# Optimization experiments

Hardware: AMD Instinct MI355X
Metric: run time of the kernel (lower is better)

## Reference

```python
import jax, jax.numpy as jnp
import numpy as np

B, S, DIM, HDIM = 8, 1024, 1024, 128
H = DIM // HDIM  # 8 heads
GN_EPS = 1e-3    # keras GroupNormalization default epsilon


def group_norm(y, gamma, beta, groups, eps=GN_EPS):
    # keras GroupNormalization on [B,S,C]: reshape to [B,S,groups,C//groups],
    # normalize over all axes except batch and group axis -> axes (1,3).
    b, s, c = y.shape
    g = y.reshape(b, s, groups, c // groups)
    mean = g.mean(axis=(1, 3), keepdims=True)
    var = g.var(axis=(1, 3), keepdims=True)
    g = (g - mean) * jax.lax.rsqrt(var + eps)
    return g.reshape(b, s, c) * gamma + beta


def setup_inputs() -> dict:
    key = jax.random.key(0)
    ks = jax.random.split(key, 7)
    x = jax.random.normal(ks[0], (B, S, DIM), dtype=jnp.float32)
    sc_h = 1.0 / np.sqrt(HDIM).astype(np.float32)
    sc_d = 1.0 / np.sqrt(DIM).astype(np.float32)
    Wq = jax.random.normal(ks[1], (H, HDIM, HDIM), dtype=jnp.float32) * sc_h
    Wk = jax.random.normal(ks[2], (H, HDIM, HDIM), dtype=jnp.float32) * sc_h
    Wv = jax.random.normal(ks[3], (H, HDIM, HDIM), dtype=jnp.float32) * sc_h
    Wg = jax.random.normal(ks[4], (DIM, DIM), dtype=jnp.float32) * sc_d
    Wo = jax.random.normal(ks[5], (DIM, DIM), dtype=jnp.float32) * sc_d
    gn_gamma = jnp.ones((DIM,), dtype=jnp.float32)
    gn_beta = jnp.zeros((DIM,), dtype=jnp.float32)
    return {"x": x, "Wq": Wq, "Wk": Wk, "Wv": Wv, "Wg": Wg, "Wo": Wo,
            "gn_gamma": gn_gamma, "gn_beta": gn_beta}


def reference(x, Wq, Wk, Wv, Wg, Wo, gn_gamma, gn_beta):
    b, s, c = x.shape
    h, hd = Wq.shape[0], Wq.shape[1]
    # gating branch: W = ReLU(x @ Wg)
    Wgate = jax.nn.relu(jnp.einsum('bsc,cd->bsd', x, Wg))
    # split channels into heads: [B,S,H,hd]
    xh = x.reshape(b, s, h, hd)
    Q = jnp.einsum('bshd,hde->bhse', xh, Wq)
    K = jnp.einsum('bshd,hde->bhse', xh, Wk)
    V = jnp.einsum('bshd,hde->bhse', xh, Wv)
    # per-head decay mask D[h,i,j] = gamma_h ** (i - j) (full, non-causal as in source)
    idx = jnp.arange(s, dtype=jnp.float32)
    gammas = 1.0 - 2.0 ** (-5.0 - jnp.arange(h, dtype=jnp.float32))  # [H]
    decay = gammas[:, None, None] ** (idx[None, :, None] - idx[None, None, :])  # [H,S,S]
    scores = jnp.einsum('bhsd,bhtd->bhst', Q, K) * decay[None]
    ret = jnp.einsum('bhst,bhtd->bhsd', scores, V)       # [B,H,S,hd]
    y = ret.transpose(0, 2, 1, 3).reshape(b, s, c)        # concat heads
    Y = group_norm(y, gn_gamma, gn_beta, groups=hd)       # groups = hdim (keras arg)
    return jnp.einsum('bsc,cd->bsd', Wgate * Y, Wo)
```

## Files before the change

kernel.cpp:

```cpp
#include <hip/hip_runtime.h>

#define BB 8
#define SS 1024
#define DD 1024
#define HH 8
#define HD 128
#define GN_EPS 1e-3f

typedef __attribute__((ext_vector_type(8))) short bf16x8;
typedef __attribute__((ext_vector_type(4))) float f32x4;

__device__ __forceinline__ short f2bf(float f) {
    unsigned u = __float_as_uint(f);
    return (short)((u + 0x7fffu + ((u >> 16) & 1u)) >> 16);
}
__device__ __forceinline__ float bf2f(short s) {
    return __uint_as_float(((unsigned)(unsigned short)s) << 16);
}

__device__ __forceinline__ void gload16(const void* g, void* l) {
    __builtin_amdgcn_global_load_lds((const __attribute__((address_space(1))) void*)g,
                                     (__attribute__((address_space(3))) void*)l, 16, 0, 0);
}

__device__ __forceinline__ void stage_tile(const short* __restrict__ G, size_t ld, int k0,
                                           short* lds, int wid, int lane) {
#pragma unroll
    for (int i = 0; i < 2; i++) {
        const int seg = wid * 2 + i;
        const int row = seg * 8 + (lane >> 3);
        const int chunk = (lane & 7) ^ (lane >> 3);
        gload16(G + (size_t)row * ld + k0 + chunk * 8, lds + seg * 512);
    }
}

__device__ __forceinline__ void gemm_tile_g(
    const short* __restrict__ A, size_t ldA,
    const short* __restrict__ B, size_t ldB,
    int K, short* As, short* Bs, f32x4 acc[4][2])
{
    const int tid = threadIdx.x, lane = tid & 63, wid = tid >> 6;
    const int wr = (wid >> 2) * 64, wc = (wid & 3) * 32;
    const int fr = lane & 15, fc = lane >> 4;
    const int rsw = fr & 7;
#pragma unroll
    for (int i = 0; i < 4; i++)
#pragma unroll
        for (int j = 0; j < 2; j++) acc[i][j] = (f32x4){0.f, 0.f, 0.f, 0.f};

    const int nt = K >> 6;
    stage_tile(A, ldA, 0, As, wid, lane);
    stage_tile(B, ldB, 0, Bs, wid, lane);
    if (nt > 1) {
        stage_tile(A, ldA, 64, As + 8192, wid, lane);
        stage_tile(B, ldB, 64, Bs + 8192, wid, lane);
    }
    for (int t = 0; t < nt; t++) {
        if (t + 1 < nt) asm volatile("s_waitcnt vmcnt(4)" ::: "memory");
        else            asm volatile("s_waitcnt vmcnt(0)" ::: "memory");
        __builtin_amdgcn_s_barrier();
        __builtin_amdgcn_sched_barrier(0);
        const int cur = t & 1;
        const short* as = As + (cur << 13);
        const short* bs = Bs + (cur << 13);
#pragma unroll
        for (int half = 0; half < 2; half++) {
            const int slot = ((half * 4 + fc) ^ rsw) << 3;
            bf16x8 af[4], bfv[2];
#pragma unroll
            for (int i = 0; i < 4; i++) af[i] = *(const bf16x8*)&as[(wr + i * 16 + fr) * 64 + slot];
#pragma unroll
            for (int j = 0; j < 2; j++) bfv[j] = *(const bf16x8*)&bs[(wc + j * 16 + fr) * 64 + slot];
#pragma unroll
            for (int i = 0; i < 4; i++)
#pragma unroll
                for (int j = 0; j < 2; j++)
                    acc[i][j] = __builtin_amdgcn_mfma_f32_16x16x32_bf16(af[i], bfv[j], acc[i][j], 0, 0, 0);
        }
        __builtin_amdgcn_sched_barrier(0);
        asm volatile("s_waitcnt lgkmcnt(0)" ::: "memory");
        __builtin_amdgcn_s_barrier();
        if (t + 2 < nt) {
            stage_tile(A, ldA, (t + 2) << 6, As + (cur << 13), wid, lane);
            stage_tile(B, ldB, (t + 2) << 6, Bs + (cur << 13), wid, lane);
        }
    }
}

__global__ __launch_bounds__(256) void prep(
    const float* __restrict__ x,
    const float* __restrict__ Wq, const float* __restrict__ Wk, const float* __restrict__ Wv,
    const float* __restrict__ Wg, const float* __restrict__ Wo,
    short* __restrict__ xb, short* __restrict__ WgT, short* __restrict__ WoT,
    short* __restrict__ Wt, float* __restrict__ sQ, float* __restrict__ sK,
    float* __restrict__ Sp)
{
    __shared__ float t[32][33];
    int bid = blockIdx.x;
    const int tid = threadIdx.x;
    if (bid < 4096) {
        const size_t i = ((size_t)bid * 256 + tid) * 8;
        float4 a = *(const float4*)&x[i];
        float4 b = *(const float4*)&x[i + 4];
        bf16x8 v;
        v[0] = f2bf(a.x); v[1] = f2bf(a.y); v[2] = f2bf(a.z); v[3] = f2bf(a.w);
        v[4] = f2bf(b.x); v[5] = f2bf(b.y); v[6] = f2bf(b.z); v[7] = f2bf(b.w);
        *(bf16x8*)&xb[i] = v;
        return;
    }
    bid -= 4096;
    if (bid < 2048) {
        const float* __restrict__ S = (bid < 1024) ? Wg : Wo;
        short* __restrict__ D = (bid < 1024) ? WgT : WoT;
        const int tb = bid & 1023;
        const int bx = (tb & 31) * 32, by = (tb >> 5) * 32;
        const int xx = tid & 31, y0 = tid >> 5;
#pragma unroll
        for (int r = 0; r < 32; r += 8) t[y0 + r][xx] = S[(size_t)(by + y0 + r) * 1024 + bx + xx];
        __syncthreads();
#pragma unroll
        for (int r = 0; r < 32; r += 8) D[(size_t)(bx + y0 + r) * 1024 + by + xx] = f2bf(t[xx][y0 + r]);
        return;
    }
    bid -= 2048;
    if (bid < 384) {
        const int ht = bid >> 4, tb = bid & 15;
        const int typ = ht >> 3, h = ht & 7;
        const float* __restrict__ W = (typ == 0 ? Wq : (typ == 1 ? Wk : Wv)) + (size_t)h * HD * HD;
        short* __restrict__ D = Wt + (size_t)ht * HD * HD;
        const int bx = (tb & 3) * 32, by = (tb >> 2) * 32;
        const int xx = tid & 31, y0 = tid >> 5;
#pragma unroll
        for (int r = 0; r < 32; r += 8) t[y0 + r][xx] = W[(by + y0 + r) * HD + bx + xx];
        __syncthreads();
#pragma unroll
        for (int r = 0; r < 32; r += 8) D[(bx + y0 + r) * HD + by + xx] = f2bf(t[xx][y0 + r]);
        return;
    }
    bid -= 384;
    if (bid < 32) {
        const int h = bid >> 2;
        const int s = (bid & 3) * 256 + tid;
        const double gamma = 1.0 - exp2((double)(-5 - h));
        const double lg = log2(gamma);
        sQ[h * SS + s] = (float)exp2(lg * (double)s);
        sK[h * SS + s] = (float)exp2(-lg * (double)s);
        return;
    }
    *(float4*)&Sp[tid * 8] = (float4){0.f, 0.f, 0.f, 0.f};
    *(float4*)&Sp[tid * 8 + 4] = (float4){0.f, 0.f, 0.f, 0.f};
}

__global__ __launch_bounds__(512) void g_qkvgate(
    const short* __restrict__ xb, const short* __restrict__ Wt, const short* __restrict__ WgT,
    const float* __restrict__ sQ, const float* __restrict__ sK,
    short* __restrict__ Qb, short* __restrict__ Ktb, short* __restrict__ Vtb,
    short* __restrict__ gateb)
{
    __shared__ short As[2 * 8192], Bs[2 * 8192];
    f32x4 acc[4][2];
    const int orig = blockIdx.x;
    const int cx = orig & 7, p = orig >> 3;
    const int tid = threadIdx.x, lane = tid & 63, wid = tid >> 6;
    const int wr = (wid >> 2) * 64, wc = (wid & 3) * 32;
    const int r0 = (lane >> 4) * 4, c = lane & 15;

    if (p < 64) {
        const int w2 = cx * 64 + p;
        const int m0 = (w2 >> 3) * 128, n0 = (w2 & 7) * 128;
        gemm_tile_g(xb + (size_t)m0 * DD, DD, WgT + (size_t)n0 * DD, DD, DD, As, Bs, acc);
#pragma unroll
        for (int i = 0; i < 4; i++)
#pragma unroll
            for (int j = 0; j < 2; j++)
#pragma unroll
                for (int r = 0; r < 4; r++)
                    gateb[(size_t)(m0 + wr + i * 16 + r0 + r) * DD + n0 + wc + j * 16 + c] =
                        f2bf(fmaxf(acc[i][j][r], 0.f));
        return;
    }
    const int w = cx * 64 + (p - 64);
    const int mt = w >> 3, h = w & 7;
    const int m0 = mt * 128;
    const int b = m0 >> 10, s0 = m0 & (SS - 1);
    const int bh = (b << 3) + h;
    const short* __restrict__ A = xb + (size_t)m0 * DD + h * HD;

    const int fr = lane & 15, fc = lane >> 4;
    const int rsw = fr & 7;

    stage_tile(A, DD, 0,  As,        wid, lane);
    stage_tile(A, DD, 64, As + 8192, wid, lane);
    stage_tile(Wt + (size_t)h * HD * HD, HD, 0, Bs, wid, lane);
    __syncthreads();

#pragma unroll
    for (int i = 0; i < 4; i++)
#pragma unroll
        for (int j = 0; j < 2; j++) acc[i][j] = (f32x4){0.f, 0.f, 0.f, 0.f};

    int sb = 0;
    for (int st = 0; st < 6; st++) {
        if (st + 1 < 6) {
            const int typn = (st + 1) >> 1, ktn = (st + 1) & 1;
            stage_tile(Wt + (size_t)(typn * 8 + h) * HD * HD, HD, ktn * 64,
                       Bs + ((sb ^ 1) << 13), wid, lane);
        }
        const int kt = st & 1;
        const short* as = As + (kt << 13);
        const short* bs = Bs + (sb << 13);
#pragma unroll
        for (int half = 0; half < 2; half++) {
            const int slot = ((half * 4 + fc) ^ rsw) << 3;
            bf16x8 af[4], bfv[2];
#pragma unroll
            for (int i = 0; i < 4; i++) af[i] = *(const bf16x8*)&as[(wr + i * 16 + fr) * 64 + slot];
#pragma unroll
            for (int j = 0; j < 2; j++) bfv[j] = *(const bf16x8*)&bs[(wc + j * 16 + fr) * 64 + slot];
#pragma unroll
            for (int i = 0; i < 4; i++)
#pragma unroll
                for (int j = 0; j < 2; j++)
                    acc[i][j] = __builtin_amdgcn_mfma_f32_16x16x32_bf16(af[i], bfv[j], acc[i][j], 0, 0, 0);
        }
        __syncthreads();
        sb ^= 1;
        if (kt == 1) {
            const int typ = st >> 1;
            if (typ == 0) {
#pragma unroll
                for (int i = 0; i < 4; i++)
#pragma unroll
                    for (int j = 0; j < 2; j++)
#pragma unroll
                        for (int r = 0; r < 4; r++) {
                            const int s = s0 + wr + i * 16 + r0 + r;
                            Qb[((size_t)bh * SS + s) * HD + wc + j * 16 + c] =
                                f2bf(acc[i][j][r] * sQ[h * SS + s]);
                        }
            } else if (typ == 1) {
                short* __restrict__ Ob = Ktb + (size_t)bh * HD * SS;
#pragma unroll
                for (int i = 0; i < 4; i++)
#pragma unroll
                    for (int j = 0; j < 2; j++) {
                        const int tb = s0 + wr + i * 16 + r0;
                        const int d = wc + j * 16 + c;
                        short4 o;
                        o.x = f2bf(acc[i][j][0] * sK[h * SS + tb + 0]);
                        o.y = f2bf(acc[i][j][1] * sK[h * SS + tb + 1]);
                        o.z = f2bf(acc[i][j][2] * sK[h * SS + tb + 2]);
                        o.w = f2bf(acc[i][j][3] * sK[h * SS + tb + 3]);
                        *(short4*)&Ob[(size_t)d * SS + tb] = o;
                    }
            } else {
                short* __restrict__ Ob = Vtb + (size_t)bh * HD * SS;
#pragma unroll
                for (int i = 0; i < 4; i++)
#pragma unroll
                    for (int j = 0; j < 2; j++) {
                        const int tb = s0 + wr + i * 16 + r0;
                        const int e = wc + j * 16 + c;
                        short4 o;
                        o.x = f2bf(acc[i][j][0]); o.y = f2bf(acc[i][j][1]);
                        o.z = f2bf(acc[i][j][2]); o.w = f2bf(acc[i][j][3]);
                        *(short4*)&Ob[(size_t)e * SS + tb] = o;
                    }
            }
#pragma unroll
            for (int i = 0; i < 4; i++)
#pragma unroll
                for (int j = 0; j < 2; j++) acc[i][j] = (f32x4){0.f, 0.f, 0.f, 0.f};
        }
    }
}

__global__ __launch_bounds__(512) void g_kv(
    const short* __restrict__ Vtb, const short* __restrict__ Ktb, float* __restrict__ Mp)
{
    __shared__ short As[2 * 8192], Bs[2 * 8192];
    f32x4 acc[4][2];
    const int orig = blockIdx.x;
    const int w = (orig & 7) * 16 + (orig >> 3);
    const int chunk = w & 1, bh = w >> 1;
    gemm_tile_g(Vtb + (size_t)bh * HD * SS + chunk * 512, SS,
                Ktb + (size_t)bh * HD * SS + chunk * 512, SS, 512, As, Bs, acc);
    const int tid = threadIdx.x, lane = tid & 63, wid = tid >> 6;
    const int wr = (wid >> 2) * 64, wc = (wid & 3) * 32;
    const int r0 = (lane >> 4) * 4, c = lane & 15;
    float* __restrict__ Ob = Mp + (size_t)w * HD * HD;
#pragma unroll
    for (int i = 0; i < 4; i++)
#pragma unroll
        for (int j = 0; j < 2; j++)
#pragma unroll
            for (int r = 0; r < 4; r++)
                Ob[(size_t)(wr + i * 16 + r0 + r) * HD + wc + j * 16 + c] = acc[i][j][r];
}

__global__ __launch_bounds__(256) void g_mredcvt(const float* __restrict__ Mp, short* __restrict__ Mtb) {
    const size_t i = ((size_t)blockIdx.x * 256 + threadIdx.x) * 8;
    const size_t bh = i >> 14, ij = i & 16383;
    const float* p = Mp + (bh * 2) * 16384 + ij;
    float s[8];
#pragma unroll
    for (int q = 0; q < 8; q++) s[q] = 0.f;
#pragma unroll
    for (int cth = 0; cth < 2; cth++) {
        float4 a = *(const float4*)&p[cth * 16384];
        float4 b = *(const float4*)&p[cth * 16384 + 4];
        s[0] += a.x; s[1] += a.y; s[2] += a.z; s[3] += a.w;
        s[4] += b.x; s[5] += b.y; s[6] += b.z; s[7] += b.w;
    }
    bf16x8 v;
#pragma unroll
    for (int q = 0; q < 8; q++) v[q] = f2bf(s[q]);
    *(bf16x8*)&Mtb[i] = v;
}

__global__ __launch_bounds__(512) void g_qm(
    const short* __restrict__ Qb, const short* __restrict__ Mtb,
    short* __restrict__ retc, float* __restrict__ Sp)
{
    __shared__ short As[2 * 8192], Bs[2 * 8192];
    f32x4 acc[4][2];
    const int orig = blockIdx.x;
    const int w = (orig & 7) * 64 + (orig >> 3);
    const int bh = w >> 3, m0 = (w & 7) * 128;
    const short* __restrict__ A = Qb + ((size_t)bh * SS + m0) * HD;
    const short* __restrict__ Bp = Mtb + (size_t)bh * HD * HD;
    const int tid = threadIdx.x, lane = tid & 63, wid = tid >> 6;
    const int wr = (wid >> 2) * 64, wc = (wid & 3) * 32;
    const int fr = lane & 15, fc = lane >> 4, rsw = fr & 7;
    const int r0 = (lane >> 4) * 4, c = lane & 15;

    stage_tile(A,  HD, 0,  As,        wid, lane);
    stage_tile(A,  HD, 64, As + 8192, wid, lane);
    stage_tile(Bp, HD, 0,  Bs,        wid, lane);
    stage_tile(Bp, HD, 64, Bs + 8192, wid, lane);
#pragma unroll
    for (int i = 0; i < 4; i++)
#pragma unroll
        for (int j = 0; j < 2; j++) acc[i][j] = (f32x4){0.f, 0.f, 0.f, 0.f};
    asm volatile("s_waitcnt vmcnt(0)" ::: "memory");
    __builtin_amdgcn_s_barrier();
    __builtin_amdgcn_sched_barrier(0);
#pragma unroll
    for (int kt = 0; kt < 2; kt++) {
        const short* as = As + (kt << 13);
        const short* bs = Bs + (kt << 13);
#pragma unroll
        for (int half = 0; half < 2; half++) {
            const int slot = ((half * 4 + fc) ^ rsw) << 3;
            bf16x8 af[4], bfv[2];
#pragma unroll
            for (int i = 0; i < 4; i++) af[i] = *(const bf16x8*)&as[(wr + i * 16 + fr) * 64 + slot];
#pragma unroll
            for (int j = 0; j < 2; j++) bfv[j] = *(const bf16x8*)&bs[(wc + j * 16 + fr) * 64 + slot];
#pragma unroll
            for (int i = 0; i < 4; i++)
#pragma unroll
                for (int j = 0; j < 2; j++)
                    acc[i][j] = __builtin_amdgcn_mfma_f32_16x16x32_bf16(af[i], bfv[j], acc[i][j], 0, 0, 0);
        }
    }
    const int b_ = bh >> 3, h_ = bh & 7;
    short* __restrict__ O = retc + ((size_t)(b_ * SS + m0)) * DD + h_ * HD;
#pragma unroll
    for (int i = 0; i < 4; i++)
#pragma unroll
        for (int j = 0; j < 2; j++)
#pragma unroll
            for (int r = 0; r < 4; r++)
                O[(size_t)(wr + i * 16 + r0 + r) * DD + wc + j * 16 + c] = f2bf(acc[i][j][r]);

    float psm[2], psq[2];
#pragma unroll
    for (int j = 0; j < 2; j++) { psm[j] = 0.f; psq[j] = 0.f; }
#pragma unroll
    for (int i = 0; i < 4; i++)
#pragma unroll
        for (int j = 0; j < 2; j++)
#pragma unroll
            for (int r = 0; r < 4; r++) {
                const float v = acc[i][j][r];
                psm[j] += v; psq[j] += v * v;
            }
    const int masks[5] = {1, 2, 4, 16, 32};
#pragma unroll
    for (int mk = 0; mk < 5; mk++) {
#pragma unroll
        for (int j = 0; j < 2; j++) {
            psm[j] += __shfl_xor(psm[j], masks[mk], 64);
            psq[j] += __shfl_xor(psq[j], masks[mk], 64);
        }
    }
    if ((lane & 7) == 0 && lane < 16) {
        const int hi = lane >> 3;
#pragma unroll
        for (int j = 0; j < 2; j++) {
            const int g = b_ * 128 + h_ * 16 + (wid & 3) * 4 + j * 2 + hi;
            atomicAdd(&Sp[g * 2 + 0], psm[j]);
            atomicAdd(&Sp[g * 2 + 1], psq[j]);
        }
    }
}

__global__ __launch_bounds__(256) void aprep(
    const short* __restrict__ gateb, const short* __restrict__ retc,
    const float* __restrict__ Sp,
    const float* __restrict__ gng, const float* __restrict__ gnb, short* __restrict__ Ab)
{
    const size_t idx = ((size_t)blockIdx.x * 256 + threadIdx.x) * 4;
    const int m = (int)(idx >> 10), cc = (int)(idx & 1023);
    const int b_ = m >> 10, g = b_ * 128 + (cc >> 3);
    const float sm = Sp[g * 2 + 0], sq = Sp[g * 2 + 1];
    const float mu = sm * (1.0f / 8192.0f);
    float var = sq * (1.0f / 8192.0f) - mu * mu;
    if (var < 0.f) var = 0.f;
    const float rs = rsqrtf(var + GN_EPS);
    short4 gv4 = *(const short4*)&gateb[idx];
    short4 rv4 = *(const short4*)&retc[idx];
    float4 gv = *(const float4*)&gng[cc];
    float4 bv = *(const float4*)&gnb[cc];
    short4 o;
    o.x = f2bf(bf2f(gv4.x) * ((bf2f(rv4.x) - mu) * rs * gv.x + bv.x));
    o.y = f2bf(bf2f(gv4.y) * ((bf2f(rv4.y) - mu) * rs * gv.y + bv.y));
    o.z = f2bf(bf2f(gv4.z) * ((bf2f(rv4.z) - mu) * rs * gv.z + bv.z));
    o.w = f2bf(bf2f(gv4.w) * ((bf2f(rv4.w) - mu) * rs * gv.w + bv.w));
    *(short4*)&Ab[idx] = o;
}

__global__ __launch_bounds__(512) void g_final(
    const short* __restrict__ Ab, const short* __restrict__ WoT, float* __restrict__ out)
{
    __shared__ short As[2 * 8192], Bs[2 * 8192];
    f32x4 acc[4][2];
    const int orig = blockIdx.x;
    const int w = (orig & 7) * 64 + (orig >> 3);
    const int m0 = (w >> 3) * 128, n0 = (w & 7) * 128;
    gemm_tile_g(Ab + (size_t)m0 * DD, DD, WoT + (size_t)n0 * DD, DD, DD, As, Bs, acc);
    const int tid = threadIdx.x, lane = tid & 63, wid = tid >> 6;
    const int wr = (wid >> 2) * 64, wc = (wid & 3) * 32;
    const int r0 = (lane >> 4) * 4, c = lane & 15;
#pragma unroll
    for (int i = 0; i < 4; i++)
#pragma unroll
        for (int j = 0; j < 2; j++)
#pragma unroll
            for (int r = 0; r < 4; r++)
                out[(size_t)(m0 + wr + i * 16 + r0 + r) * DD + n0 + wc + j * 16 + c] = acc[i][j][r];
}

extern "C" void kernel_launch(void* const* d_in, const int* in_sizes, int n_in,
                              void* d_out, int out_size, void* d_ws, size_t ws_size,
                              hipStream_t stream)
{
    const float* x   = (const float*)d_in[0];
    const float* Wq  = (const float*)d_in[1];
    const float* Wk  = (const float*)d_in[2];
    const float* Wv  = (const float*)d_in[3];
    const float* Wg  = (const float*)d_in[4];
    const float* Wo  = (const float*)d_in[5];
    const float* gng = (const float*)d_in[6];
    const float* gnb = (const float*)d_in[7];
    float* out = (float*)d_out;

    char* ws = (char*)d_ws;
    size_t off = 0;
    auto alloc = [&](size_t bytes) -> void* {
        void* p = ws + off;
        off += (bytes + 255) & ~(size_t)255;
        return p;
    };
    const size_t NE = (size_t)BB * SS * DD;
    float*  sQ    = (float*)alloc((size_t)HH * SS * sizeof(float));
    float*  sK    = (float*)alloc((size_t)HH * SS * sizeof(float));
    short*  xb    = (short*)alloc(NE * sizeof(short));
    short*  WgT   = (short*)alloc((size_t)DD * DD * sizeof(short));
    short*  WoT   = (short*)alloc((size_t)DD * DD * sizeof(short));
    short*  Wt    = (short*)alloc((size_t)24 * HD * HD * sizeof(short));
    short*  Qb    = (short*)alloc(NE * sizeof(short));
    short*  Ktb   = (short*)alloc(NE * sizeof(short));
    short*  Vtb   = (short*)alloc(NE * sizeof(short));
    short*  retc  = (short*)alloc(NE * sizeof(short));
    short*  gateb = (short*)alloc(NE * sizeof(short));
    short*  Ab    = (short*)alloc(NE * sizeof(short));
    float*  Mp    = (float*)alloc((size_t)128 * HD * HD * sizeof(float));
    short*  Mtb   = (short*)alloc((size_t)64 * HD * HD * sizeof(short));
    float*  Sp    = (float*)alloc((size_t)1024 * 2 * sizeof(float));

    prep<<<dim3(6561), 256, 0, stream>>>(x, Wq, Wk, Wv, Wg, Wo, xb, WgT, WoT, Wt, sQ, sK, Sp);
    g_qkvgate<<<dim3(1024), 512, 0, stream>>>(xb, Wt, WgT, sQ, sK, Qb, Ktb, Vtb, gateb);
    g_kv<<<dim3(128), 512, 0, stream>>>(Vtb, Ktb, Mp);
    g_mredcvt<<<dim3(512), 256, 0, stream>>>(Mp, Mtb);
    g_qm<<<dim3(512), 512, 0, stream>>>(Qb, Mtb, retc, Sp);
    aprep<<<dim3(8192), 256, 0, stream>>>(gateb, retc, Sp, gng, gnb, Ab);
    g_final<<<dim3(512), 512, 0, stream>>>(Ab, WoT, out);
}
```

Before: 112.3 us.

## Use 256x128 output tiles with K=32 stages for gate and output GEMMs

Adds a new GEMM tile routine that computes 256x128 output tiles per block, with 8 waves each owning a 64x64 sub-tile (4x4 MFMA accumulators) and double-buffered K-steps of 32 using swizzled LDS staging. The gate GEMM in g_qkvgate and the final output GEMM now use it, halving their block counts (1024->768 and 512->256 launches). The aim is more MFMA work per LDS fragment load and less redundant global traffic per output element. The cost is more accumulator registers per thread, more barrier trips per K, and fewer blocks, which on a 256-CU part can leave units underfilled.

```diff
diff --git a/kernel.cpp b/kernel.cpp
--- a/kernel.cpp
+++ b/kernel.cpp
@@ -83,6 +83,71 @@
         if (t + 2 < nt) {
             stage_tile(A, ldA, (t + 2) << 6, As + (cur << 13), wid, lane);
             stage_tile(B, ldB, (t + 2) << 6, Bs + (cur << 13), wid, lane);
+        }
+    }
+}
+
+__device__ __forceinline__ void stage_A32(const short* __restrict__ G, size_t ld, int k0,
+                                          short* lds, int wid, int lane) {
+#pragma unroll
+    for (int i = 0; i < 2; i++) {
+        const int row = wid * 32 + i * 16 + (lane >> 2);
+        const int chunk = (lane & 3) ^ ((row >> 1) & 3);
+        gload16(G + (size_t)row * ld + k0 + chunk * 8, lds + wid * 1024 + i * 512);
+    }
+}
+__device__ __forceinline__ void stage_B32(const short* __restrict__ G, size_t ld, int k0,
+                                          short* lds, int wid, int lane) {
+    const int row = wid * 16 + (lane >> 2);
+    const int chunk = (lane & 3) ^ ((row >> 1) & 3);
+    gload16(G + (size_t)row * ld + k0 + chunk * 8, lds + wid * 512);
+}
+
+__device__ __forceinline__ void gemm_tile_n(
+    const short* __restrict__ A, size_t ldA,
+    const short* __restrict__ B, size_t ldB,
+    int K, short* As, short* Bs, f32x4 acc[4][4])
+{
+    const int tid = threadIdx.x, lane = tid & 63, wid = tid >> 6;
+    const int wr = (wid >> 1) * 64, wc = (wid & 1) * 64;
+    const int fr = lane & 15, fc = lane >> 4;
+    const int slot = (fc ^ ((fr >> 1) & 3)) << 3;
+#pragma unroll
+    for (int i = 0; i < 4; i++)
+#pragma unroll
+        for (int j = 0; j < 4; j++) acc[i][j] = (f32x4){0.f, 0.f, 0.f, 0.f};
+
+    const int nt = K >> 5;
+    stage_A32(A, ldA, 0, As, wid, lane);
+    stage_B32(B, ldB, 0, Bs, wid, lane);
+    if (nt > 1) {
+        stage_A32(A, ldA, 32, As + 8192, wid, lane);
+        stage_B32(B, ldB, 32, Bs + 4096, wid, lane);
+    }
+    for (int t = 0; t < nt; t++) {
+        if (t + 1 < nt) asm volatile("s_waitcnt vmcnt(3)" ::: "memory");
+        else            asm volatile("s_waitcnt vmcnt(0)" ::: "memory");
+        __builtin_amdgcn_s_barrier();
+        __builtin_amdgcn_sched_barrier(0);
+        const int cur = t & 1;
+        const short* as = As + (cur << 13);
+        const short* bs = Bs + (cur << 12);
+        bf16x8 af[4], bfv[4];
+#pragma unroll
+        for (int i = 0; i < 4; i++) af[i] = *(const bf16x8*)&as[(wr + i * 16 + fr) * 32 + slot];
+#pragma unroll
+        for (int j = 0; j < 4; j++) bfv[j] = *(const bf16x8*)&bs[(wc + j * 16 + fr) * 32 + slot];
+#pragma unroll
+        for (int i = 0; i < 4; i++)
+#pragma unroll
+            for (int j = 0; j < 4; j++)
+                acc[i][j] = __builtin_amdgcn_mfma_f32_16x16x32_bf16(af[i], bfv[j], acc[i][j], 0, 0, 0);
+        __builtin_amdgcn_sched_barrier(0);
+        asm volatile("s_waitcnt lgkmcnt(0)" ::: "memory");
+        __builtin_amdgcn_s_barrier();
+        if (t + 2 < nt) {
+            stage_A32(A, ldA, (t + 2) << 5, As + (cur << 13), wid, lane);
+            stage_B32(B, ldB, (t + 2) << 5, Bs + (cur << 12), wid, lane);
         }
     }
 }
@@ -158,34 +223,35 @@
     short* __restrict__ gateb)
 {
     __shared__ short As[2 * 8192], Bs[2 * 8192];
-    f32x4 acc[4][2];
     const int orig = blockIdx.x;
     const int cx = orig & 7, p = orig >> 3;
     const int tid = threadIdx.x, lane = tid & 63, wid = tid >> 6;
-    const int wr = (wid >> 2) * 64, wc = (wid & 3) * 32;
     const int r0 = (lane >> 4) * 4, c = lane & 15;
 
-    if (p < 64) {
-        const int w2 = cx * 64 + p;
-        const int m0 = (w2 >> 3) * 128, n0 = (w2 & 7) * 128;
-        gemm_tile_g(xb + (size_t)m0 * DD, DD, WgT + (size_t)n0 * DD, DD, DD, As, Bs, acc);
+    if (p < 32) {
+        f32x4 acc[4][4];
+        const int w2 = cx * 32 + p;
+        const int m0 = (w2 >> 3) * 256, n0 = (w2 & 7) * 128;
+        gemm_tile_n(xb + (size_t)m0 * DD, DD, WgT + (size_t)n0 * DD, DD, DD, As, Bs, acc);
+        const int wr = (wid >> 1) * 64, wc = (wid & 1) * 64;
 #pragma unroll
         for (int i = 0; i < 4; i++)
 #pragma unroll
-            for (int j = 0; j < 2; j++)
+            for (int j = 0; j < 4; j++)
 #pragma unroll
                 for (int r = 0; r < 4; r++)
                     gateb[(size_t)(m0 + wr + i * 16 + r0 + r) * DD + n0 + wc + j * 16 + c] =
                         f2bf(fmaxf(acc[i][j][r], 0.f));
         return;
     }
-    const int w = cx * 64 + (p - 64);
+    f32x4 acc[4][2];
+    const int w = cx * 64 + (p - 32);
     const int mt = w >> 3, h = w & 7;
     const int m0 = mt * 128;
     const int b = m0 >> 10, s0 = m0 & (SS - 1);
     const int bh = (b << 3) + h;
     const short* __restrict__ A = xb + (size_t)m0 * DD + h * HD;
-
+    const int wr = (wid >> 2) * 64, wc = (wid & 3) * 32;
     const int fr = lane & 15, fc = lane >> 4;
     const int rsw = fr & 7;
 
@@ -434,19 +500,19 @@
 __global__ __launch_bounds__(512) void g_final(
     const short* __restrict__ Ab, const short* __restrict__ WoT, float* __restrict__ out)
 {
-    __shared__ short As[2 * 8192], Bs[2 * 8192];
-    f32x4 acc[4][2];
+    __shared__ short As[2 * 8192], Bs[2 * 4096];
+    f32x4 acc[4][4];
     const int orig = blockIdx.x;
-    const int w = (orig & 7) * 64 + (orig >> 3);
-    const int m0 = (w >> 3) * 128, n0 = (w & 7) * 128;
-    gemm_tile_g(Ab + (size_t)m0 * DD, DD, WoT + (size_t)n0 * DD, DD, DD, As, Bs, acc);
+    const int w = (orig & 7) * 32 + (orig >> 3);
+    const int m0 = (w >> 3) * 256, n0 = (w & 7) * 128;
+    gemm_tile_n(Ab + (size_t)m0 * DD, DD, WoT + (size_t)n0 * DD, DD, DD, As, Bs, acc);
     const int tid = threadIdx.x, lane = tid & 63, wid = tid >> 6;
-    const int wr = (wid >> 2) * 64, wc = (wid & 3) * 32;
+    const int wr = (wid >> 1) * 64, wc = (wid & 1) * 64;
     const int r0 = (lane >> 4) * 4, c = lane & 15;
 #pragma unroll
     for (int i = 0; i < 4; i++)
 #pragma unroll
-        for (int j = 0; j < 2; j++)
+        for (int j = 0; j < 4; j++)
 #pragma unroll
             for (int r = 0; r < 4; r++)
                 out[(size_t)(m0 + wr + i * 16 + r0 + r) * DD + n0 + wc + j * 16 + c] = acc[i][j][r];
@@ -491,10 +557,10 @@
     float*  Sp    = (float*)alloc((size_t)1024 * 2 * sizeof(float));
 
     prep<<<dim3(6561), 256, 0, stream>>>(x, Wq, Wk, Wv, Wg, Wo, xb, WgT, WoT, Wt, sQ, sK, Sp);
-    g_qkvgate<<<dim3(1024), 512, 0, stream>>>(xb, Wt, WgT, sQ, sK, Qb, Ktb, Vtb, gateb);
+    g_qkvgate<<<dim3(768), 512, 0, stream>>>(xb, Wt, WgT, sQ, sK, Qb, Ktb, Vtb, gateb);
     g_kv<<<dim3(128), 512, 0, stream>>>(Vtb, Ktb, Mp);
     g_mredcvt<<<dim3(512), 256, 0, stream>>>(Mp, Mtb);
     g_qm<<<dim3(512), 512, 0, stream>>>(Qb, Mtb, retc, Sp);
     aprep<<<dim3(8192), 256, 0, stream>>>(gateb, retc, Sp, gng, gnb, Ab);
-    g_final<<<dim3(512), 512, 0, stream>>>(Ab, WoT, out);
-}
+    g_final<<<dim3(256), 512, 0, stream>>>(Ab, WoT, out);
+}
```

Measured after the change: 117.4 us. 4.6% more time.
